# Optimization experiments

Measured on AMD Instinct MI355X. Metric: run time of the kernel, lower is better.

## Reference

```python
import jax, jax.numpy as jnp
import numpy as np

EPS = 1e-5
K_UP = 5      # k_upsample
SCALE = 2

def _conv(x, w, pad):
    # NCHW conv, no bias
    return jax.lax.conv_general_dilated(
        x, w, window_strides=(1, 1), padding=((pad, pad), (pad, pad)),
        dimension_numbers=('NCHW', 'OIHW', 'NCHW'))

def _bn(x, gamma, beta):
    # train-mode BatchNorm2d forward: batch stats over (N,H,W), biased var
    m = x.mean(axis=(0, 2, 3), keepdims=True)
    v = x.var(axis=(0, 2, 3), keepdims=True)
    xn = (x - m) * jax.lax.rsqrt(v + EPS)
    return xn * gamma[None, :, None, None] + beta[None, :, None, None]

def _pixel_shuffle(x, r):
    b, c, h, w = x.shape
    co = c // (r * r)
    x = x.reshape(b, co, r, r, h, w)
    x = x.transpose(0, 1, 4, 2, 5, 3)  # b, co, h, r, w, r
    return x.reshape(b, co, h * r, w * r)

def setup_inputs() -> dict:
    key = jax.random.key(0)
    ks = jax.random.split(key, 3)
    b, c, h, w = 8, 128, 64, 64
    mid = 64
    return {
        'x': jax.random.normal(ks[0], (b, c, h, w), jnp.float32),
        'comp_w': jax.random.normal(ks[1], (mid, c, 1, 1), jnp.float32) * (1.0 / np.sqrt(c)),
        'comp_g': jnp.ones((mid,), jnp.float32),
        'comp_b': jnp.zeros((mid,), jnp.float32),
        'enc_w': jax.random.normal(ks[2], ((K_UP * SCALE) ** 2, mid, 3, 3), jnp.float32) * (1.0 / np.sqrt(mid * 9)),
        'enc_g': jnp.ones(((K_UP * SCALE) ** 2,), jnp.float32),
        'enc_b': jnp.zeros(((K_UP * SCALE) ** 2,), jnp.float32),
    }

def reference(x, comp_w, comp_g, comp_b, enc_w, enc_g, enc_b):
    b, c, h, w = x.shape
    hm, wm = h * SCALE, w * SCALE
    # --- kernel prediction branch ---
    t = jax.nn.silu(_bn(_conv(x, comp_w, 0), comp_g, comp_b))        # [b,64,h,w]
    t = _bn(_conv(t, enc_w, 1), enc_g, enc_b)                        # [b,100,h,w] (act=False)
    t = _pixel_shuffle(t, SCALE)                                     # [b,25,hm,wm]
    wgt = jax.nn.softmax(t, axis=1)                                  # [b,25,hm,wm]
    # --- feature reassembly branch ---
    x_up = jnp.repeat(jnp.repeat(x, SCALE, axis=2), SCALE, axis=3)   # nearest upsample
    pad = (K_UP // 2) * SCALE  # = 4, preserves hm x wm with dilation=SCALE
    xp = jnp.pad(x_up, ((0, 0), (0, 0), (pad, pad), (pad, pad)))
    # unfold: kernel K_UP, dilation SCALE -> [b, c, 25, hm, wm], taps in (kh, kw) order
    patches = jnp.stack(
        [xp[:, :, dy * SCALE:dy * SCALE + hm, dx * SCALE:dx * SCALE + wm]
         for dy in range(K_UP) for dx in range(K_UP)], axis=2)
    # content-aware weighted sum over the 25 taps
    return jnp.einsum('bkhw,bckhw->bchw', wgt, patches)
```

## Files before the change

### kernel.cpp

```cpp
#include <hip/hip_runtime.h>
#include <hip/hip_bf16.h>
#include <math.h>

#define C_   128
#define HW_  4096
#define OC_  100
#define NSTAT_ 32768.0f

typedef __bf16 bf16x8 __attribute__((ext_vector_type(8)));
typedef __bf16 bf16x4 __attribute__((ext_vector_type(4)));
typedef float  f32x4  __attribute__((ext_vector_type(4)));

__global__ __launch_bounds__(256, 4) void k_conv1(const float* __restrict__ x,
                                                  const float* __restrict__ w,
                                                  const float* __restrict__ wenc,
                                                  __bf16* __restrict__ t1c,
                                                  float* __restrict__ csum,
                                                  float* __restrict__ csq,
                                                  __bf16* __restrict__ wprep) {
    __shared__ __bf16 xt[64 * 128];
    __shared__ __bf16 wt[64 * 128];
    __shared__ float sS[64], sQ[64];

    int blk = blockIdx.x;
    int b = blk & 7;
    int chunk = blk >> 3;
    int px0 = chunk * 64;
    int tid = threadIdx.x;
    if (tid < 64) { sS[tid] = 0.f; sQ[tid] = 0.f; }

    if (blk < 63) {
#pragma unroll
        for (int u = 0; u < 4; ++u) {
            int idx = blk * 1024 + u * 256 + tid;
            int oc = idx / 576, k = idx - oc * 576;
            int tap = k >> 6, ic = k & 63;
            wprep[idx] = (oc < OC_) ? (__bf16)wenc[((size_t)oc * 64 + ic) * 9 + tap]
                                    : (__bf16)0.f;
        }
    }

#pragma unroll
    for (int it = 0; it < 8; ++it) {
        int j = it * 256 + tid;
        int oc = j >> 5, f = j & 31;
        float4 v = *(const float4*)(w + (size_t)oc * 128 + f * 4);
        int blki = (f >> 1) ^ (oc & 15);
        bf16x4 st;
        st[0] = (__bf16)v.x; st[1] = (__bf16)v.y; st[2] = (__bf16)v.z; st[3] = (__bf16)v.w;
        *(bf16x4*)&wt[oc * 128 + blki * 8 + (f & 1) * 4] = st;
    }
#pragma unroll
    for (int it = 0; it < 2; ++it) {
        int j = it * 256 + tid;
        int px4 = (j & 15) * 4, icq = j >> 4;
        const float* xp = x + ((size_t)b * C_ + icq * 4) * HW_ + px0 + px4;
        float4 v0 = *(const float4*)(xp);
        float4 v1 = *(const float4*)(xp + HW_);
        float4 v2 = *(const float4*)(xp + 2 * HW_);
        float4 v3 = *(const float4*)(xp + 3 * HW_);
        float r0[4] = {v0.x, v0.y, v0.z, v0.w};
        float r1[4] = {v1.x, v1.y, v1.z, v1.w};
        float r2_[4] = {v2.x, v2.y, v2.z, v2.w};
        float r3[4] = {v3.x, v3.y, v3.z, v3.w};
#pragma unroll
        for (int r2 = 0; r2 < 4; ++r2) {
            int px = px4 + r2;
            int blki = (icq >> 1) ^ (px & 15);
            bf16x4 st;
            st[0] = (__bf16)r0[r2]; st[1] = (__bf16)r1[r2];
            st[2] = (__bf16)r2_[r2]; st[3] = (__bf16)r3[r2];
            *(bf16x4*)&xt[px * 128 + blki * 8 + (icq & 1) * 4] = st;
        }
    }
    __syncthreads();

    int lane = tid & 63, wv = tid >> 6;
    int p = lane & 15, q = lane >> 4;

    f32x4 acc[4];
#pragma unroll
    for (int n = 0; n < 4; ++n) acc[n] = (f32x4){0.f, 0.f, 0.f, 0.f};

#pragma unroll
    for (int kk = 0; kk < 4; ++kk) {
        int blki = (kk * 4 + q) ^ p;
        bf16x8 a = *(const bf16x8*)&xt[(wv * 16 + p) * 128 + blki * 8];
#pragma unroll
        for (int n = 0; n < 4; ++n) {
            bf16x8 bb = *(const bf16x8*)&wt[(n * 16 + p) * 128 + blki * 8];
            acc[n] = __builtin_amdgcn_mfma_f32_16x16x32_bf16(a, bb, acc[n], 0, 0, 0);
        }
    }

    __bf16* t1b = t1c + ((size_t)b * HW_ + px0 + wv * 16) * 64;
#pragma unroll
    for (int n = 0; n < 4; ++n) {
        float s = 0.f, qq = 0.f;
#pragma unroll
        for (int rg = 0; rg < 4; ++rg) {
            float v = acc[n][rg];
            t1b[(size_t)(q * 4 + rg) * 64 + n * 16 + p] = (__bf16)v;
            s += v; qq += v * v;
        }
        s += __shfl_down(s, 32, 64);  s += __shfl_down(s, 16, 64);
        qq += __shfl_down(qq, 32, 64); qq += __shfl_down(qq, 16, 64);
        if (lane < 16) {
            atomicAdd(&sS[n * 16 + p], s);
            atomicAdd(&sQ[n * 16 + p], qq);
        }
    }
    __syncthreads();
    if (tid < 64) {
        atomicAdd(&csum[tid], sS[tid]);
        atomicAdd(&csq[tid], sQ[tid]);
    }
}

__global__ __launch_bounds__(256, 4) void k_conv3(const __bf16* __restrict__ t1c,
                                                  const __bf16* __restrict__ wprep,
                                                  const float* __restrict__ csum,
                                                  const float* __restrict__ csq,
                                                  const float* __restrict__ cg,
                                                  const float* __restrict__ cb,
                                                  float* __restrict__ t2c,
                                                  float* __restrict__ esum,
                                                  float* __restrict__ esq) {
    __shared__ __bf16 xt[10 * 10 * 72];
    __shared__ __bf16 bt[2][112 * 32];
    __shared__ float lsc[64], lsh[64];
    __shared__ float esuml[112], esql[112];

    int blk = blockIdx.x;
    int b = blk & 7;
    int tile = blk >> 3;
    int ty0 = (tile >> 3) * 8, tx0 = (tile & 7) * 8;
    int tid = threadIdx.x;
    if (tid < 112) { esuml[tid] = 0.f; esql[tid] = 0.f; }
    if (tid >= 128 && tid < 192) {
        int c = tid - 128;
        float invN = 1.0f / NSTAT_;
        float m = csum[c] * invN;
        float v = csq[c] * invN - m * m;
        float rs = rsqrtf(v + 1e-5f);
        float sc = cg[c] * rs;
        lsc[c] = sc;
        lsh[c] = cb[c] - m * sc;
    }
    __syncthreads();

    {
        int oc = tid >> 2, part = tid & 3;
        *(bf16x8*)&bt[0][oc * 32 + part * 8] =
            *(const bf16x8*)(wprep + (size_t)oc * 576 + part * 8);
        if (tid < 192) {
            int c1 = tid + 256;
            int oc1 = c1 >> 2, p1 = c1 & 3;
            *(bf16x8*)&bt[0][oc1 * 32 + p1 * 8] =
                *(const bf16x8*)(wprep + (size_t)oc1 * 576 + p1 * 8);
        }
    }

    const __bf16* tb = t1c + (size_t)b * HW_ * 64;
#pragma unroll
    for (int it = 0; it < 7; ++it) {
        int idx = it * 256 + tid;
        if (idx < 1600) {
            int pxi = idx >> 4, f4 = idx & 15;
            int yy = pxi / 10, xx = pxi - yy * 10;
            int gy = ty0 + yy - 1, gx = tx0 + xx - 1;
            float o0 = 0.f, o1 = 0.f, o2 = 0.f, o3 = 0.f;
            if (gy >= 0 && gy < 64 && gx >= 0 && gx < 64) {
                bf16x4 v = *(const bf16x4*)(tb + ((size_t)(gy << 6) + gx) * 64 + f4 * 4);
                float4 sc = *(const float4*)(lsc + f4 * 4);
                float4 sh = *(const float4*)(lsh + f4 * 4);
                float u;
                u = fmaf((float)v[0], sc.x, sh.x); o0 = u / (1.f + __expf(-u));
                u = fmaf((float)v[1], sc.y, sh.y); o1 = u / (1.f + __expf(-u));
                u = fmaf((float)v[2], sc.z, sh.z); o2 = u / (1.f + __expf(-u));
                u = fmaf((float)v[3], sc.w, sh.w); o3 = u / (1.f + __expf(-u));
            }
            bf16x4 st;
            st[0] = (__bf16)o0; st[1] = (__bf16)o1; st[2] = (__bf16)o2; st[3] = (__bf16)o3;
            *(bf16x4*)&xt[pxi * 72 + f4 * 4] = st;
        }
    }
    __syncthreads();

    int lane = tid & 63, wv = tid >> 6;
    int p = lane & 15, q = lane >> 4;
    int ya = 2 * wv + (p >> 3), xa = p & 7;
    int soc = tid >> 2, spart = tid & 3;
    int soc1 = (tid + 256) >> 2, spart1 = (tid + 256) & 3;

    f32x4 acc[7];
#pragma unroll
    for (int n = 0; n < 7; ++n) acc[n] = (f32x4){0.f, 0.f, 0.f, 0.f};

#pragma unroll
    for (int kk = 0; kk < 18; ++kk) {
        const int cur = kk & 1;
        bf16x8 r0, r1;
        if (kk < 17) {
            r0 = *(const bf16x8*)(wprep + (size_t)soc * 576 + (kk + 1) * 32 + spart * 8);
            if (tid < 192)
                r1 = *(const bf16x8*)(wprep + (size_t)soc1 * 576 + (kk + 1) * 32 + spart1 * 8);
        }
        const int tap = kk >> 1, ich = (kk & 1) * 32;
        const int ky = tap / 3, kx = tap - ky * 3;
        bf16x8 a0 = *(const bf16x8*)&xt[((ya + ky) * 10 + xa + kx) * 72 + ich + q * 8];
#pragma unroll
        for (int n = 0; n < 7; ++n) {
            bf16x8 bb = *(const bf16x8*)&bt[cur][(n * 16 + p) * 32 + q * 8];
            acc[n] = __builtin_amdgcn_mfma_f32_16x16x32_bf16(a0, bb, acc[n], 0, 0, 0);
        }
        if (kk < 17) {
            *(bf16x8*)&bt[1 - cur][soc * 32 + spart * 8] = r0;
            if (tid < 192)
                *(bf16x8*)&bt[1 - cur][soc1 * 32 + spart1 * 8] = r1;
            __syncthreads();
        }
    }

    float* t2b = t2c + (size_t)b * HW_ * 112;
#pragma unroll
    for (int n = 0; n < 7; ++n) {
        float s = 0.f, qq = 0.f;
#pragma unroll
        for (int rg = 0; rg < 4; ++rg) {
            int mp = q * 4 + rg;
            int y = ty0 + 2 * wv + (mp >> 3), xo = tx0 + (mp & 7);
            float v = acc[n][rg];
            t2b[((size_t)y * 64 + xo) * 112 + n * 16 + p] = v;
            s += v; qq += v * v;
        }
        s += __shfl_down(s, 32, 64);  s += __shfl_down(s, 16, 64);
        qq += __shfl_down(qq, 32, 64); qq += __shfl_down(qq, 16, 64);
        if (lane < 16) {
            atomicAdd(&esuml[n * 16 + lane], s);
            atomicAdd(&esql[n * 16 + lane], qq);
        }
    }
    __syncthreads();
    if (tid < 112) {
        atomicAdd(&esum[tid], esuml[tid]);
        atomicAdd(&esq[tid], esql[tid]);
    }
}

__global__ __launch_bounds__(256, 4) void k_carafe(const float* __restrict__ x,
                                                   const float* __restrict__ t2c,
                                                   const float* __restrict__ esum,
                                                   const float* __restrict__ esq,
                                                   const float* __restrict__ eg,
                                                   const float* __restrict__ eb,
                                                   float* __restrict__ out) {
    __shared__ float xt[2][160 * 20];
    __shared__ float esc[112], esh[112];

    int blk = blockIdx.x;
    int b = blk & 7;
    int r = blk >> 3;
    int tile = r & 63;
    int chalf = r >> 6;
    int tx0 = (tile & 3) * 16, ty0 = (tile >> 2) * 4;
    int tid = threadIdx.x;
    if (tid < 112) {
        float invN = 1.0f / NSTAT_;
        float m = esum[tid] * invN;
        float v = esq[tid] * invN - m * m;
        float rs = rsqrtf(v + 1e-5f);
        float sc = (tid < OC_) ? eg[tid] * rs : 0.f;
        esc[tid] = sc;
        esh[tid] = (tid < OC_) ? eb[tid] - m * sc : 0.f;
    }
    __syncthreads();

    int s = tid & 3, px = tid >> 2;
    int pxx = px & 15, py = px >> 4;
    int iy = ty0 + py, jx = tx0 + pxx;

    float wgt[25];
    {
        const float* t2p = t2c + ((size_t)((b << 12) + (iy << 6) + jx)) * 112 + s;
        float mx = -1e30f;
#pragma unroll
        for (int k = 0; k < 25; ++k) {
            float l = fmaf(t2p[k * 4], esc[4 * k + s], esh[4 * k + s]);
            wgt[k] = l;
            mx = fmaxf(mx, l);
        }
        float sum = 0.f;
#pragma unroll
        for (int k = 0; k < 25; ++k) {
            float e = __expf(wgt[k] - mx);
            wgt[k] = e;
            sum += e;
        }
        float inv = 1.f / sum;
#pragma unroll
        for (int k = 0; k < 25; ++k) wgt[k] *= inv;
    }

    const float* xb = x + (size_t)b * C_ * HW_;
    int i0 = iy * 2 + (s >> 1), j0 = jx * 2 + (s & 1);
    float* op = out + (size_t)b * C_ * 16384 + (size_t)i0 * 128 + j0;

    int sidx[3], sgy[3], sgx[3], sc4[3];
#pragma unroll
    for (int it = 0; it < 3; ++it) {
        int idx = it * 256 + tid;
        sidx[it] = idx;
        int c4 = idx / 160;
        int r2 = idx - c4 * 160;
        int yy = r2 / 20, xx = r2 - yy * 20;
        sgy[it] = ty0 - 2 + yy;
        sgx[it] = tx0 - 2 + xx;
        sc4[it] = c4;
    }

#pragma unroll
    for (int it = 0; it < 3; ++it) {
        if (sidx[it] < 640) {
            int gy = sgy[it], gx = sgx[it];
            f32x4 st = {0.f, 0.f, 0.f, 0.f};
            if (gy >= 0 && gy < 64 && gx >= 0 && gx < 64) {
                size_t base = (size_t)(chalf * 64 + sc4[it] * 4) * HW_ + (gy << 6) + gx;
                st[0] = xb[base];
                st[1] = xb[base + HW_];
                st[2] = xb[base + 2 * HW_];
                st[3] = xb[base + 3 * HW_];
            }
            int r2 = sidx[it] - sc4[it] * 160;
            *(f32x4*)&xt[0][r2 * 20 + sc4[it] * 4] = st;
        }
    }

#pragma unroll
    for (int stage = 0; stage < 4; ++stage) {
        int cur = stage & 1;
        int cbase = chalf * 64 + stage * 16;
        f32x4 pf[3];
        if (stage < 3) {
#pragma unroll
            for (int it = 0; it < 3; ++it) {
                if (sidx[it] < 640) {
                    int gy = sgy[it], gx = sgx[it];
                    f32x4 st = {0.f, 0.f, 0.f, 0.f};
                    if (gy >= 0 && gy < 64 && gx >= 0 && gx < 64) {
                        size_t base = (size_t)(cbase + 16 + sc4[it] * 4) * HW_ + (gy << 6) + gx;
                        st[0] = xb[base];
                        st[1] = xb[base + HW_];
                        st[2] = xb[base + 2 * HW_];
                        st[3] = xb[base + 3 * HW_];
                    }
                    pf[it] = st;
                }
            }
        }
        __syncthreads();

        float acc[16];
#pragma unroll
        for (int e = 0; e < 16; ++e) acc[e] = 0.f;
#pragma unroll
        for (int dy = 0; dy < 5; ++dy)
#pragma unroll
            for (int dx = 0; dx < 5; ++dx) {
                int pxi = (py + dy) * 20 + pxx + dx;
                float wk = wgt[dy * 5 + dx];
#pragma unroll
                for (int c4 = 0; c4 < 4; ++c4) {
                    f32x4 xv = *(const f32x4*)&xt[cur][pxi * 20 + c4 * 4];
                    acc[c4 * 4 + 0] = fmaf(wk, xv[0], acc[c4 * 4 + 0]);
                    acc[c4 * 4 + 1] = fmaf(wk, xv[1], acc[c4 * 4 + 1]);
                    acc[c4 * 4 + 2] = fmaf(wk, xv[2], acc[c4 * 4 + 2]);
                    acc[c4 * 4 + 3] = fmaf(wk, xv[3], acc[c4 * 4 + 3]);
                }
            }
#pragma unroll
        for (int e = 0; e < 16; ++e)
            op[(size_t)(cbase + e) * 16384] = acc[e];

        if (stage < 3) {
#pragma unroll
            for (int it = 0; it < 3; ++it) {
                if (sidx[it] < 640) {
                    int r2 = sidx[it] - sc4[it] * 160;
                    *(f32x4*)&xt[1 - cur][r2 * 20 + sc4[it] * 4] = pf[it];
                }
            }
        }
    }
}

extern "C" void kernel_launch(void* const* d_in, const int* in_sizes, int n_in,
                              void* d_out, int out_size, void* d_ws, size_t ws_size,
                              hipStream_t stream) {
    const float* x      = (const float*)d_in[0];
    const float* comp_w = (const float*)d_in[1];
    const float* comp_g = (const float*)d_in[2];
    const float* comp_b = (const float*)d_in[3];
    const float* enc_w  = (const float*)d_in[4];
    const float* enc_g  = (const float*)d_in[5];
    const float* enc_b  = (const float*)d_in[6];
    float* out = (float*)d_out;

    float* ws = (float*)d_ws;
    __bf16* t1c = (__bf16*)ws;
    float* t2c  = ws + 1048576;
    float* st   = ws + 1048576 + 3670016;
    float* csum = st;
    float* csq  = st + 64;
    float* esum = st + 128;
    float* esq  = st + 240;
    __bf16* wprep = (__bf16*)(st + 352);

    hipMemsetAsync(st, 0, 352 * sizeof(float), stream);
    k_conv1<<<512, 256, 0, stream>>>(x, comp_w, enc_w, t1c, csum, csq, wprep);
    k_conv3<<<512, 256, 0, stream>>>(t1c, wprep, csum, csq, comp_g, comp_b, t2c, esum, esq);
    k_carafe<<<1024, 256, 0, stream>>>(x, t2c, esum, esq, enc_g, enc_b, out);
}
```

Before: 152.7 us.

## Enlarge CARAFE tile and compute two sub-pixels per thread for reuse

The CARAFE kernel now covers a 16x8 low-res tile per block (twice as tall) and has each thread produce two horizontally adjacent output sub-pixels that share the same input window. Every shared-memory load of x now feeds two FMA streams, and outputs are written as float2. This halves the grid, amortizes the halo load over more pixels, and roughly halves LDS reads per FMA. In exchange it raises register pressure (50 weights, 32 accumulators), relaxes launch bounds to 2 blocks per SM, uses more LDS, and keeps the stage loop rolled.

```diff
diff --git a/kernel.cpp b/kernel.cpp
--- a/kernel.cpp
+++ b/kernel.cpp
@@ -248,22 +248,22 @@
     }
 }
 
-__global__ __launch_bounds__(256, 4) void k_carafe(const float* __restrict__ x,
+__global__ __launch_bounds__(256, 2) void k_carafe(const float* __restrict__ x,
                                                    const float* __restrict__ t2c,
                                                    const float* __restrict__ esum,
                                                    const float* __restrict__ esq,
                                                    const float* __restrict__ eg,
                                                    const float* __restrict__ eb,
                                                    float* __restrict__ out) {
-    __shared__ float xt[2][160 * 20];
+    __shared__ float xt[2][240 * 20];
     __shared__ float esc[112], esh[112];
 
     int blk = blockIdx.x;
     int b = blk & 7;
     int r = blk >> 3;
-    int tile = r & 63;
-    int chalf = r >> 6;
-    int tx0 = (tile & 3) * 16, ty0 = (tile >> 2) * 4;
+    int tile = r & 31;
+    int chalf = r >> 5;
+    int tx0 = (tile & 3) * 16, ty0 = (tile >> 2) * 8;
     int tid = threadIdx.x;
     if (tid < 112) {
         float invN = 1.0f / NSTAT_;
@@ -276,52 +276,57 @@
     }
     __syncthreads();
 
-    int s = tid & 3, px = tid >> 2;
+    int t0 = tid & 1, px = tid >> 1;
     int pxx = px & 15, py = px >> 4;
     int iy = ty0 + py, jx = tx0 + pxx;
 
-    float wgt[25];
+    float wA[25], wB[25];
     {
-        const float* t2p = t2c + ((size_t)((b << 12) + (iy << 6) + jx)) * 112 + s;
-        float mx = -1e30f;
+        const float* t2p = t2c + ((size_t)((b << 12) + (iy << 6) + jx)) * 112 + 2 * t0;
+        int cA = 2 * t0, cB = 2 * t0 + 1;
+        float mxA = -1e30f, mxB = -1e30f;
 #pragma unroll
         for (int k = 0; k < 25; ++k) {
-            float l = fmaf(t2p[k * 4], esc[4 * k + s], esh[4 * k + s]);
-            wgt[k] = l;
-            mx = fmaxf(mx, l);
-        }
-        float sum = 0.f;
+            float2 v = *(const float2*)(t2p + 4 * k);
+            float lA = fmaf(v.x, esc[4 * k + cA], esh[4 * k + cA]);
+            float lB = fmaf(v.y, esc[4 * k + cB], esh[4 * k + cB]);
+            wA[k] = lA; wB[k] = lB;
+            mxA = fmaxf(mxA, lA); mxB = fmaxf(mxB, lB);
+        }
+        float sA = 0.f, sB = 0.f;
 #pragma unroll
         for (int k = 0; k < 25; ++k) {
-            float e = __expf(wgt[k] - mx);
-            wgt[k] = e;
-            sum += e;
-        }
-        float inv = 1.f / sum;
-#pragma unroll
-        for (int k = 0; k < 25; ++k) wgt[k] *= inv;
+            float eA = __expf(wA[k] - mxA);
+            float eB = __expf(wB[k] - mxB);
+            wA[k] = eA; wB[k] = eB;
+            sA += eA; sB += eB;
+        }
+        float iA = 1.f / sA, iB = 1.f / sB;
+#pragma unroll
+        for (int k = 0; k < 25; ++k) { wA[k] *= iA; wB[k] *= iB; }
     }
 
     const float* xb = x + (size_t)b * C_ * HW_;
-    int i0 = iy * 2 + (s >> 1), j0 = jx * 2 + (s & 1);
-    float* op = out + (size_t)b * C_ * 16384 + (size_t)i0 * 128 + j0;
-
-    int sidx[3], sgy[3], sgx[3], sc4[3];
-#pragma unroll
-    for (int it = 0; it < 3; ++it) {
+    int i0 = iy * 2 + t0;
+    float* op = out + (size_t)b * C_ * 16384 + (size_t)i0 * 128 + jx * 2;
+
+    int sidx[4], sgy[4], sgx[4], sr2[4], sc4[4];
+#pragma unroll
+    for (int it = 0; it < 4; ++it) {
         int idx = it * 256 + tid;
         sidx[it] = idx;
-        int c4 = idx / 160;
-        int r2 = idx - c4 * 160;
+        int c4 = idx / 240;
+        int r2 = idx - c4 * 240;
         int yy = r2 / 20, xx = r2 - yy * 20;
+        sr2[it] = r2;
+        sc4[it] = c4;
         sgy[it] = ty0 - 2 + yy;
         sgx[it] = tx0 - 2 + xx;
-        sc4[it] = c4;
-    }
-
-#pragma unroll
-    for (int it = 0; it < 3; ++it) {
-        if (sidx[it] < 640) {
+    }
+
+#pragma unroll
+    for (int it = 0; it < 4; ++it) {
+        if (sidx[it] < 960) {
             int gy = sgy[it], gx = sgx[it];
             f32x4 st = {0.f, 0.f, 0.f, 0.f};
             if (gy >= 0 && gy < 64 && gx >= 0 && gx < 64) {
@@ -331,20 +336,19 @@
                 st[2] = xb[base + 2 * HW_];
                 st[3] = xb[base + 3 * HW_];
             }
-            int r2 = sidx[it] - sc4[it] * 160;
-            *(f32x4*)&xt[0][r2 * 20 + sc4[it] * 4] = st;
-        }
-    }
-
-#pragma unroll
+            *(f32x4*)&xt[0][sr2[it] * 20 + sc4[it] * 4] = st;
+        }
+    }
+
+#pragma unroll 1
     for (int stage = 0; stage < 4; ++stage) {
         int cur = stage & 1;
         int cbase = chalf * 64 + stage * 16;
-        f32x4 pf[3];
+        f32x4 pf[4];
         if (stage < 3) {
 #pragma unroll
-            for (int it = 0; it < 3; ++it) {
-                if (sidx[it] < 640) {
+            for (int it = 0; it < 4; ++it) {
+                if (sidx[it] < 960) {
                     int gy = sgy[it], gx = sgx[it];
                     f32x4 st = {0.f, 0.f, 0.f, 0.f};
                     if (gy >= 0 && gy < 64 && gx >= 0 && gx < 64) {
@@ -360,35 +364,40 @@
         }
         __syncthreads();
 
-        float acc[16];
-#pragma unroll
-        for (int e = 0; e < 16; ++e) acc[e] = 0.f;
+        float accA[16], accB[16];
+#pragma unroll
+        for (int e = 0; e < 16; ++e) { accA[e] = 0.f; accB[e] = 0.f; }
 #pragma unroll
         for (int dy = 0; dy < 5; ++dy)
 #pragma unroll
             for (int dx = 0; dx < 5; ++dx) {
-                int pxi = (py + dy) * 20 + pxx + dx;
-                float wk = wgt[dy * 5 + dx];
+                int pos = (py + dy) * 20 + pxx + dx;
+                float a = wA[dy * 5 + dx], bw = wB[dy * 5 + dx];
 #pragma unroll
                 for (int c4 = 0; c4 < 4; ++c4) {
-                    f32x4 xv = *(const f32x4*)&xt[cur][pxi * 20 + c4 * 4];
-                    acc[c4 * 4 + 0] = fmaf(wk, xv[0], acc[c4 * 4 + 0]);
-                    acc[c4 * 4 + 1] = fmaf(wk, xv[1], acc[c4 * 4 + 1]);
-                    acc[c4 * 4 + 2] = fmaf(wk, xv[2], acc[c4 * 4 + 2]);
-                    acc[c4 * 4 + 3] = fmaf(wk, xv[3], acc[c4 * 4 + 3]);
+                    f32x4 xv = *(const f32x4*)&xt[cur][pos * 20 + c4 * 4];
+                    accA[c4 * 4 + 0] = fmaf(a, xv[0], accA[c4 * 4 + 0]);
+                    accA[c4 * 4 + 1] = fmaf(a, xv[1], accA[c4 * 4 + 1]);
+                    accA[c4 * 4 + 2] = fmaf(a, xv[2], accA[c4 * 4 + 2]);
+                    accA[c4 * 4 + 3] = fmaf(a, xv[3], accA[c4 * 4 + 3]);
+                    accB[c4 * 4 + 0] = fmaf(bw, xv[0], accB[c4 * 4 + 0]);
+                    accB[c4 * 4 + 1] = fmaf(bw, xv[1], accB[c4 * 4 + 1]);
+                    accB[c4 * 4 + 2] = fmaf(bw, xv[2], accB[c4 * 4 + 2]);
+                    accB[c4 * 4 + 3] = fmaf(bw, xv[3], accB[c4 * 4 + 3]);
                 }
             }
 #pragma unroll
-        for (int e = 0; e < 16; ++e)
-            op[(size_t)(cbase + e) * 16384] = acc[e];
+        for (int e = 0; e < 16; ++e) {
+            float2 st2;
+            st2.x = accA[e]; st2.y = accB[e];
+            *(float2*)&op[(size_t)(cbase + e) * 16384] = st2;
+        }
 
         if (stage < 3) {
 #pragma unroll
-            for (int it = 0; it < 3; ++it) {
-                if (sidx[it] < 640) {
-                    int r2 = sidx[it] - sc4[it] * 160;
-                    *(f32x4*)&xt[1 - cur][r2 * 20 + sc4[it] * 4] = pf[it];
-                }
+            for (int it = 0; it < 4; ++it) {
+                if (sidx[it] < 960)
+                    *(f32x4*)&xt[1 - cur][sr2[it] * 20 + sc4[it] * 4] = pf[it];
             }
         }
     }
@@ -419,5 +428,5 @@
     hipMemsetAsync(st, 0, 352 * sizeof(float), stream);
     k_conv1<<<512, 256, 0, stream>>>(x, comp_w, enc_w, t1c, csum, csq, wprep);
     k_conv3<<<512, 256, 0, stream>>>(t1c, wprep, csum, csq, comp_g, comp_b, t2c, esum, esq);
-    k_carafe<<<1024, 256, 0, stream>>>(x, t2c, esum, esq, enc_g, enc_b, out);
+    k_carafe<<<512, 256, 0, stream>>>(x, t2c, esum, esq, enc_g, enc_b, out);
 }
```

Measured after the change: 169.0 us. 10.6% more time.
